# Optimization experiments

Hardware: AMD Instinct MI355X
Metric: run time of the kernel (lower is better)

Reference implementation:

```python
import jax, jax.numpy as jnp
import numpy as np

LN_EPS = 1e-5

def _dwconv(x, w, b, pad, groups):
    # x: (B,C,H,W), w: (C_out, C_in/groups, kh, kw)
    y = jax.lax.conv_general_dilated(
        x, w, window_strides=(1, 1),
        padding=[(pad[0], pad[0]), (pad[1], pad[1])],
        dimension_numbers=('NCHW', 'OIHW', 'NCHW'),
        feature_group_count=groups)
    return y + b[None, :, None, None]

def _ln(x, g, b):
    m = x.mean(-1, keepdims=True)
    v = ((x - m) ** 2).mean(-1, keepdims=True)
    return (x - m) / jnp.sqrt(v + LN_EPS) * g + b

def _lin(x, w, b):
    return x @ w.T + b

def setup_inputs() -> dict:
    key = jax.random.key(0)
    ks = jax.random.split(key, 24)
    f32 = jnp.float32
    W = lambda k, s: (jax.random.normal(k, s, f32) * 0.02)
    inp = {
        'feat': jax.random.normal(ks[0], (16, 64, 256, 256), f32),
        'head': jax.random.normal(ks[1], (16, 1, 64), f32),
        'pred': jax.random.normal(ks[2], (16, 1, 128, 128), f32),
        # dwconv Conv2d(1,1,3,3)
        'dw_w': W(ks[3], (1, 1, 3, 3)), 'dw_b': jnp.zeros((1,), f32),
        # InceptionDWConv2d(64): gc=8
        'inc_hw_w': W(ks[4], (8, 1, 3, 3)), 'inc_hw_b': jnp.zeros((8,), f32),
        'inc_w_w': W(ks[5], (8, 1, 1, 11)), 'inc_w_b': jnp.zeros((8,), f32),
        'inc_h_w': W(ks[6], (8, 1, 11, 1)), 'inc_h_b': jnp.zeros((8,), f32),
        # linear layers
        'pt_w': W(ks[7], (128, 64)), 'pt_b': jnp.zeros((128,), f32),
        'ht_w': W(ks[8], (128, 64)), 'ht_b': jnp.zeros((128,), f32),
        'pg_w': W(ks[9], (64, 64)), 'pg_b': jnp.zeros((64,), f32),
        'hg_w': W(ks[10], (64, 64)), 'hg_b': jnp.zeros((64,), f32),
        'fc_w': W(ks[11], (64, 64)), 'fc_b': jnp.zeros((64,), f32),
        # layernorms
        'pni_g': jnp.ones((64,), f32), 'pni_b': jnp.zeros((64,), f32),
        'hni_g': jnp.ones((64,), f32), 'hni_b': jnp.zeros((64,), f32),
        'pno_g': jnp.ones((64,), f32), 'pno_b': jnp.zeros((64,), f32),
        'hno_g': jnp.ones((64,), f32), 'hno_b': jnp.zeros((64,), f32),
        'fcn_g': jnp.ones((64,), f32), 'fcn_b': jnp.zeros((64,), f32),
    }
    return inp

def reference(feat, head, pred,
              dw_w, dw_b, inc_hw_w, inc_hw_b, inc_w_w, inc_w_b, inc_h_w, inc_h_b,
              pt_w, pt_b, ht_w, ht_b, pg_w, pg_b, hg_w, hg_b, fc_w, fc_b,
              pni_g, pni_b, hni_g, hni_b, pno_g, pno_b, hno_g, hno_b, fcn_g, fcn_b):
    bs, num_classes = head.shape[:2]
    C = 64  # in_channels == feat_channels
    B, _, Hp, Wp = pred.shape
    H, Wd = 2 * Hp, 2 * Wp
    # bilinear upsample x2 (align_corners=False == half-pixel)
    pred = jax.image.resize(pred, (B, num_classes, H, Wd), method='bilinear')
    pred = jax.nn.sigmoid(pred)
    pred_minus = 1.0 - jax.nn.sigmoid(pred)  # sigmoid applied twice, as in source
    pred_add = pred * pred_minus + pred
    pred_conv = _dwconv(pred_add, dw_w, dw_b, (1, 1), groups=1)
    pred = pred + pred_conv
    # InceptionDWConv2d: split (40,8,8,8)
    x_id, x_hw, x_w, x_h = feat[:, :40], feat[:, 40:48], feat[:, 48:56], feat[:, 56:64]
    feat = jnp.concatenate([
        x_id,
        _dwconv(x_hw, inc_hw_w, inc_hw_b, (1, 1), groups=8),
        _dwconv(x_w, inc_w_w, inc_w_b, (0, 5), groups=8),
        _dwconv(x_h, inc_h_w, inc_h_b, (5, 0), groups=8),
    ], axis=1)
    # FFT-based assembly: (bs,nc,1,H,W) x (bs,1,C,H,W)
    pred_fft = jnp.fft.rfft2(pred[:, :, None])
    feat_fft = jnp.fft.rfft2(feat[:, None])
    assemble = jnp.fft.irfft2(pred_fft * feat_fft, s=(H, Wd))  # (bs,nc,C,H,W)
    assemble = assemble.sum(axis=(3, 4))  # (bs,nc,C)
    # head: (bs,nc,C*k*k) -> (bs,nc,k*k,C)
    head = head.reshape(bs, num_classes, C, -1).transpose(0, 1, 3, 2)
    assemble = assemble.reshape(-1, C)
    bs_num = assemble.shape[0]
    pred_feat = _lin(assemble, pt_w, pt_b)  # (bs_num, 128)
    pred_feat_in = pred_feat[:, :C]
    pred_feat_out = pred_feat[:, -C:]
    head_feat = _lin(head.reshape(bs_num, -1, C), ht_w, ht_b)  # (bs_num, kk, 128)
    head_feat_in = head_feat[..., :C]
    head_feat_out = head_feat[..., -C:]
    gate_feat = head_feat_in * pred_feat_in[:, None, :]
    head_gate = jax.nn.sigmoid(_ln(_lin(gate_feat, hg_w, hg_b), hni_g, hni_b))
    pred_gate = jax.nn.sigmoid(_ln(_lin(gate_feat, pg_w, pg_b), pni_g, pni_b))
    head_feat_out = _ln(head_feat_out, hno_g, hno_b)
    pred_feat_out = _ln(pred_feat_out, pno_g, pno_b)
    update_head = pred_gate * pred_feat_out[:, None, :] + head_gate * head_feat_out
    update_head = _lin(update_head, fc_w, fc_b)
    update_head = jax.nn.relu(_ln(update_head, fcn_g, fcn_b))
    update_head = update_head.reshape(bs, num_classes, -1, C).transpose(0, 1, 3, 2)
    return update_head.reshape(bs, num_classes, C, 1, 1)
```

## Files before the change

kernel.cpp:

```cpp
#include <hip/hip_runtime.h>
#include <math.h>


typedef float nfloat4 __attribute__((ext_vector_type(4)));

__global__ __launch_bounds__(256) void k_main(
    const float* __restrict__ feat,
    const float* __restrict__ pred,
    const float* __restrict__ w_hw, const float* __restrict__ b_hw,
    const float* __restrict__ w_w,  const float* __restrict__ b_w,
    const float* __restrict__ w_h,  const float* __restrict__ b_h,
    float* __restrict__ sumF,
    float* __restrict__ predpart)
{
  const int tid  = threadIdx.x;
  const int lane = tid & 63;
  const int wid  = tid >> 6;

  if (blockIdx.x >= 128) {
    const int plane = blockIdx.x - 128;
    const int c = plane & 63;
    const nfloat4* x4 = reinterpret_cast<const nfloat4*>(feat) + (size_t)plane * 16384;

    if (c < 40) {
      __shared__ float red[4];
      float ax = 0.f, ay = 0.f, az = 0.f, aw = 0.f;
      #pragma unroll 8
      for (int it = 0; it < 64; ++it) {
        const nfloat4 v = __builtin_nontemporal_load(&x4[it * 256 + tid]);
        ax += v.x; ay += v.y; az += v.z; aw += v.w;
      }
      float tot = (ax + ay) + (az + aw);
      #pragma unroll
      for (int off = 32; off; off >>= 1) tot += __shfl_down(tot, off, 64);
      if (lane == 0) red[wid] = tot;
      __syncthreads();
      if (tid == 0) sumF[plane] = (red[0] + red[1]) + (red[2] + red[3]);
      return;
    }

    __shared__ float s_red[4];
    __shared__ float s_rs[10];
    __shared__ float s_cs4[4][10];
    __shared__ float s_k[4];

    float ax = 0.f, ay = 0.f, az = 0.f, aw = 0.f;
    float rowA = 0.f, rowB = 0.f, rowC = 0.f, rowD = 0.f;
    float v0x = 0.f, v0w = 0.f, v63x = 0.f, v63w = 0.f;
    #pragma unroll 8
    for (int it = 0; it < 64; ++it) {
      const nfloat4 v = __builtin_nontemporal_load(&x4[it * 256 + tid]);
      ax += v.x; ay += v.y; az += v.z; aw += v.w;
      const float s4 = (v.x + v.y) + (v.z + v.w);
      rowA += (it == 0)  ? s4 : 0.f;
      rowB += (it == 1)  ? s4 : 0.f;
      rowC += (it == 62) ? s4 : 0.f;
      rowD += (it == 63) ? s4 : 0.f;
      if (it == 0)  { v0x = v.x;  v0w = v.w; }
      if (it == 63) { v63x = v.x; v63w = v.w; }
    }
    float tot = (ax + ay) + (az + aw);
    float r0 = rowA, r1 = rowB, r2 = rowC, r3 = rowD;
    #pragma unroll
    for (int off = 32; off; off >>= 1) {
      tot += __shfl_down(tot, off, 64);
      r0  += __shfl_down(r0, off, 64);
      r1  += __shfl_down(r1, off, 64);
      r2  += __shfl_down(r2, off, 64);
      r3  += __shfl_down(r3, off, 64);
    }
    if (lane == 0) {
      s_red[wid] = tot;
      s_rs[wid] = r0;
      if (wid == 0) s_rs[4] = r1;
      if (wid == 3) s_rs[5] = r2;
      s_rs[6 + wid] = r3;
      s_cs4[wid][0] = ax; s_cs4[wid][1] = ay; s_cs4[wid][2] = az; s_cs4[wid][3] = aw;
    }
    if (lane == 1)  { s_cs4[wid][4] = ax; }
    if (lane == 62) { s_cs4[wid][5] = aw; }
    if (lane == 63) { s_cs4[wid][6] = ax; s_cs4[wid][7] = ay;
                      s_cs4[wid][8] = az; s_cs4[wid][9] = aw; }
    if (tid == 0)   s_k[0] = v0x;
    if (tid == 63)  s_k[1] = v0w;
    if (tid == 192) s_k[2] = v63x;
    if (tid == 255) s_k[3] = v63w;
    __syncthreads();

    if (tid == 0) {
      const float T = (s_red[0] + s_red[1]) + (s_red[2] + s_red[3]);
      float cs[10];
      #pragma unroll
      for (int k = 0; k < 10; ++k)
        cs[k] = (s_cs4[0][k] + s_cs4[1][k]) + (s_cs4[2][k] + s_cs4[3][k]);
      const float k00 = s_k[0], k01 = s_k[1], k10 = s_k[2], k11 = s_k[3];

      float topP[6], botP[6], leftP[6], rightP[6];
      topP[0] = botP[0] = leftP[0] = rightP[0] = 0.f;
      #pragma unroll
      for (int k = 0; k < 5; ++k) {
        topP[k+1]   = topP[k]   + s_rs[k];
        botP[k+1]   = botP[k]   + s_rs[9-k];
        leftP[k+1]  = leftP[k]  + cs[k];
        rightP[k+1] = rightP[k] + cs[9-k];
      }
      auto rect = [&](int du, int dv) -> float {
        float r = T;
        if (du > 0) r -= topP[du]; else if (du < 0) r -= botP[-du];
        if (dv > 0) r -= leftP[dv]; else if (dv < 0) r -= rightP[-dv];
        if (du > 0 && dv > 0) r += k00;
        else if (du > 0 && dv < 0) r += k01;
        else if (du < 0 && dv > 0) r += k10;
        else if (du < 0 && dv < 0) r += k11;
        return r;
      };
      float S;
      if (c < 48) {
        const int g = c - 40; const float* w = w_hw + g * 9;
        S = 65536.f * b_hw[g];
        #pragma unroll
        for (int u = 0; u < 3; ++u)
          #pragma unroll
          for (int v = 0; v < 3; ++v)
            S += w[u*3+v] * rect(u-1, v-1);
      } else if (c < 56) {
        const int g = c - 48; const float* w = w_w + g * 11;
        S = 65536.f * b_w[g];
        #pragma unroll
        for (int v = 0; v < 11; ++v) S += w[v] * rect(0, v-5);
      } else {
        const int g = c - 56; const float* w = w_h + g * 11;
        S = 65536.f * b_h[g];
        #pragma unroll
        for (int u = 0; u < 11; ++u) S += w[u] * rect(u-5, 0);
      }
      sumF[plane] = S;
    }
    return;
  }

  __shared__ float red[12];
  const int pb = blockIdx.x;
  const int b  = pb >> 3;
  const int g  = pb & 7;
  const int j  = tid;
  const float* src = pred + (size_t)b * 16384;

  const int kj = j >> 1;
  int c0, c1; float wc0, wc1;
  if ((j & 1) == 0) { c0 = (kj > 0) ? kj - 1 : 0; c1 = kj; wc0 = 0.25f; wc1 = 0.75f; }
  else              { c0 = kj; c1 = (kj < 127) ? kj + 1 : 127; wc0 = 0.75f; wc1 = 0.25f; }

  float accP = 0.f, accT = 0.f, accC = 0.f, redge = 0.f, cornA = 0.f, cornB = 0.f;
  const int i0 = g * 32;
  #pragma unroll 4
  for (int i = i0; i < i0 + 32; ++i) {
    const int ki = i >> 1;
    int r0, r1; float wr0, wr1;
    if ((i & 1) == 0) { r0 = (ki > 0) ? ki - 1 : 0; r1 = ki; wr0 = 0.25f; wr1 = 0.75f; }
    else              { r0 = ki; r1 = (ki < 127) ? ki + 1 : 127; wr0 = 0.75f; wr1 = 0.25f; }
    const float v = wr0 * (wc0 * src[r0*128 + c0] + wc1 * src[r0*128 + c1])
                  + wr1 * (wc0 * src[r1*128 + c0] + wc1 * src[r1*128 + c1]);
    const float p  = 1.f / (1.f + expf(-v));
    const float pm = 1.f - 1.f / (1.f + expf(-p));
    const float pa = p * pm + p;
    accP += p; accT += pa;
    if (j == 0 || j == 255) accC += pa;
    if (i == 0 || i == 255) {
      redge += pa;
      if (j == 0)   cornA = pa;
      if (j == 255) cornB = pa;
    }
  }
  float a0 = accP, a1 = accT, a2 = redge;
  #pragma unroll
  for (int off = 32; off; off >>= 1) {
    a0 += __shfl_down(a0, off, 64);
    a1 += __shfl_down(a1, off, 64);
    a2 += __shfl_down(a2, off, 64);
  }
  if (lane == 0) { red[wid] = a0; red[4 + wid] = a1; red[8 + wid] = a2; }
  __syncthreads();
  float* pp = predpart + pb * 8;
  if (tid == 0) {
    pp[0] = (red[0] + red[1]) + (red[2] + red[3]);
    pp[1] = (red[4] + red[5]) + (red[6] + red[7]);
    pp[4] = (red[8] + red[9]) + (red[10] + red[11]);
    pp[2] = accC; pp[5] = cornA;
  }
  if (tid == 255) { pp[3] = accC; pp[6] = cornB; }
}

__device__ __forceinline__ float wsum64(float v) {
  #pragma unroll
  for (int off = 32; off; off >>= 1) v += __shfl_xor(v, off, 64);
  return v;
}

__global__ __launch_bounds__(128) void k_tail(
    const float* __restrict__ sumF, const float* __restrict__ predpart,
    const float* __restrict__ head,
    const float* __restrict__ dw_w, const float* __restrict__ dw_b,
    const float* __restrict__ pt_w, const float* __restrict__ pt_b,
    const float* __restrict__ ht_w, const float* __restrict__ ht_b,
    const float* __restrict__ pg_w, const float* __restrict__ pg_b,
    const float* __restrict__ hg_w, const float* __restrict__ hg_b,
    const float* __restrict__ fc_w, const float* __restrict__ fc_b,
    const float* __restrict__ pni_g, const float* __restrict__ pni_b,
    const float* __restrict__ hni_g, const float* __restrict__ hni_b,
    const float* __restrict__ pno_g, const float* __restrict__ pno_b,
    const float* __restrict__ hno_g, const float* __restrict__ hno_b,
    const float* __restrict__ fcn_g, const float* __restrict__ fcn_b,
    float* __restrict__ out)
{
  const int b = blockIdx.x;
  const int t = threadIdx.x;
  const int ln = t & 63;
  __shared__ float a[64], hd[64], pf[128], hf[128], gate[64];
  __shared__ float hgate[64], pgate[64], pfo[64], hfo[64], upd[64];
  __shared__ float s_sP;

  const float sf = (t < 64) ? sumF[b * 64 + t] : 0.f;
  if (t < 64) hd[t] = head[b * 64 + t];

  if (t == 0) {
    const float* pp = predpart + b * 64;
    float P = 0.f, T = 0.f, C0 = 0.f, C255 = 0.f;
    #pragma unroll
    for (int g = 0; g < 8; ++g) {
      P += pp[g*8 + 0]; T += pp[g*8 + 1]; C0 += pp[g*8 + 2]; C255 += pp[g*8 + 3];
    }
    const float R0 = pp[0*8 + 4], R255 = pp[7*8 + 4];
    const float k00 = pp[0*8 + 5], k01 = pp[0*8 + 6];
    const float k10 = pp[7*8 + 5], k11 = pp[7*8 + 6];
    auto rect = [&](int du, int dv) -> float {
      float r = T;
      if (du > 0) r -= R0; else if (du < 0) r -= R255;
      if (dv > 0) r -= C0; else if (dv < 0) r -= C255;
      if (du > 0 && dv > 0) r += k00;
      else if (du > 0 && dv < 0) r += k01;
      else if (du < 0 && dv > 0) r += k10;
      else if (du < 0 && dv < 0) r += k11;
      return r;
    };
    float S = P + 65536.f * dw_b[0];
    #pragma unroll
    for (int u = 0; u < 3; ++u)
      #pragma unroll
      for (int v = 0; v < 3; ++v)
        S += dw_w[u*3+v] * rect(u-1, v-1);
    s_sP = S;
  }
  __syncthreads();
  if (t < 64) a[t] = sf * s_sP;
  __syncthreads();

  {
    const float4* ptw4 = reinterpret_cast<const float4*>(pt_w) + t * 16;
    const float4* htw4 = reinterpret_cast<const float4*>(ht_w) + t * 16;
    const float4* a4  = reinterpret_cast<const float4*>(a);
    const float4* hd4 = reinterpret_cast<const float4*>(hd);
    float sp = pt_b[t], sh = ht_b[t];
    #pragma unroll
    for (int kk = 0; kk < 16; ++kk) {
      const float4 wp = ptw4[kk], wh = htw4[kk];
      const float4 av = a4[kk],  hv = hd4[kk];
      sp += av.x*wp.x + av.y*wp.y + av.z*wp.z + av.w*wp.w;
      sh += hv.x*wh.x + hv.y*wh.y + hv.z*wh.z + hv.w*wh.w;
    }
    pf[t] = sp; hf[t] = sh;
  }
  __syncthreads();
  if (t < 64) gate[t] = hf[t] * pf[t];
  __syncthreads();

  float glin;
  {
    const float* gw = (t < 64) ? hg_w : pg_w;
    float s = (t < 64) ? hg_b[ln] : pg_b[ln];
    const float4* gw4 = reinterpret_cast<const float4*>(gw) + ln * 16;
    const float4* g4  = reinterpret_cast<const float4*>(gate);
    #pragma unroll
    for (int kk = 0; kk < 16; ++kk) {
      const float4 w = gw4[kk], gv = g4[kk];
      s += gv.x*w.x + gv.y*w.y + gv.z*w.z + gv.w*w.w;
    }
    glin = s;
  }
  {
    const float m = wsum64(glin) * (1.f/64.f);
    const float d = glin - m;
    const float var = wsum64(d*d) * (1.f/64.f);
    const float* g  = (t < 64) ? hni_g : pni_g;
    const float* bb = (t < 64) ? hni_b : pni_b;
    const float y = d / sqrtf(var + 1e-5f) * g[ln] + bb[ln];
    const float sg = 1.f / (1.f + expf(-y));
    if (t < 64) hgate[ln] = sg; else pgate[ln] = sg;
  }
  {
    const float x = (t < 64) ? hf[64 + ln] : pf[64 + ln];
    const float m = wsum64(x) * (1.f/64.f);
    const float d = x - m;
    const float var = wsum64(d*d) * (1.f/64.f);
    const float* g  = (t < 64) ? hno_g : pno_g;
    const float* bb = (t < 64) ? hno_b : pno_b;
    const float y = d / sqrtf(var + 1e-5f) * g[ln] + bb[ln];
    if (t < 64) hfo[ln] = y; else pfo[ln] = y;
  }
  __syncthreads();
  if (t < 64) upd[t] = pgate[t] * pfo[t] + hgate[t] * hfo[t];
  __syncthreads();
  if (t < 64) {
    const float4* fw4 = reinterpret_cast<const float4*>(fc_w) + t * 16;
    const float4* u4  = reinterpret_cast<const float4*>(upd);
    float s = fc_b[t];
    #pragma unroll
    for (int kk = 0; kk < 16; ++kk) {
      const float4 w = fw4[kk], uv = u4[kk];
      s += uv.x*w.x + uv.y*w.y + uv.z*w.z + uv.w*w.w;
    }
    const float m = wsum64(s) * (1.f/64.f);
    const float d = s - m;
    const float var = wsum64(d*d) * (1.f/64.f);
    const float y = d / sqrtf(var + 1e-5f) * fcn_g[t] + fcn_b[t];
    out[b * 64 + t] = fmaxf(y, 0.f);
  }
}

extern "C" void kernel_launch(void* const* d_in, const int* in_sizes, int n_in,
                              void* d_out, int out_size, void* d_ws, size_t ws_size,
                              hipStream_t stream) {
  (void)in_sizes; (void)n_in; (void)out_size; (void)ws_size;
  const float* feat     = (const float*)d_in[0];
  const float* head     = (const float*)d_in[1];
  const float* pred     = (const float*)d_in[2];
  const float* dw_w     = (const float*)d_in[3];
  const float* dw_b     = (const float*)d_in[4];
  const float* inc_hw_w = (const float*)d_in[5];
  const float* inc_hw_b = (const float*)d_in[6];
  const float* inc_w_w  = (const float*)d_in[7];
  const float* inc_w_b  = (const float*)d_in[8];
  const float* inc_h_w  = (const float*)d_in[9];
  const float* inc_h_b  = (const float*)d_in[10];
  const float* pt_w  = (const float*)d_in[11];
  const float* pt_b  = (const float*)d_in[12];
  const float* ht_w  = (const float*)d_in[13];
  const float* ht_b  = (const float*)d_in[14];
  const float* pg_w  = (const float*)d_in[15];
  const float* pg_b  = (const float*)d_in[16];
  const float* hg_w  = (const float*)d_in[17];
  const float* hg_b  = (const float*)d_in[18];
  const float* fc_w  = (const float*)d_in[19];
  const float* fc_b  = (const float*)d_in[20];
  const float* pni_g = (const float*)d_in[21];
  const float* pni_b = (const float*)d_in[22];
  const float* hni_g = (const float*)d_in[23];
  const float* hni_b = (const float*)d_in[24];
  const float* pno_g = (const float*)d_in[25];
  const float* pno_b = (const float*)d_in[26];
  const float* hno_g = (const float*)d_in[27];
  const float* hno_b = (const float*)d_in[28];
  const float* fcn_g = (const float*)d_in[29];
  const float* fcn_b = (const float*)d_in[30];

  float* out      = (float*)d_out;
  float* sumF     = (float*)d_ws;
  float* predpart = sumF + 1024;

  k_main<<<1152, 256, 0, stream>>>(feat, pred,
                                   inc_hw_w, inc_hw_b, inc_w_w, inc_w_b,
                                   inc_h_w, inc_h_b, sumF, predpart);
  k_tail<<<16, 128, 0, stream>>>(sumF, predpart, head, dw_w, dw_b,
                                 pt_w, pt_b, ht_w, ht_b,
                                 pg_w, pg_b, hg_w, hg_b, fc_w, fc_b,
                                 pni_g, pni_b, hni_g, hni_b,
                                 pno_g, pno_b, hno_g, hno_b,
                                 fcn_g, fcn_b, out);
}
```

Measured before the change: 53.66 us.

## Fuse tail into main kernel via per-batch last-block-done atomic counter

Merges the two kernels into one launch. Each block increments a per-batch counter when it finishes, and the last of the 72 blocks for that batch runs the small MLP tail, reading partial results with atomic loads. This removes the second kernel launch and the gap between kernels. In exchange it adds a memset launch for the counters, atomics and fences in every block, and the tail now runs serially at the end of the last block for each batch.

```diff
diff --git a/kernel.cpp b/kernel.cpp
--- a/kernel.cpp
+++ b/kernel.cpp
@@ -4,201 +4,22 @@
 
 typedef float nfloat4 __attribute__((ext_vector_type(4)));
 
-__global__ __launch_bounds__(256) void k_main(
+__device__ __forceinline__ float aload(const float* p) {
+  return __hip_atomic_load(p, __ATOMIC_RELAXED, __HIP_MEMORY_SCOPE_AGENT);
+}
+
+__device__ __forceinline__ float wsum64(float v) {
+  #pragma unroll
+  for (int off = 32; off; off >>= 1) v += __shfl_xor(v, off, 64);
+  return v;
+}
+
+__global__ __launch_bounds__(256) void k_all(
     const float* __restrict__ feat,
     const float* __restrict__ pred,
     const float* __restrict__ w_hw, const float* __restrict__ b_hw,
     const float* __restrict__ w_w,  const float* __restrict__ b_w,
     const float* __restrict__ w_h,  const float* __restrict__ b_h,
-    float* __restrict__ sumF,
-    float* __restrict__ predpart)
-{
-  const int tid  = threadIdx.x;
-  const int lane = tid & 63;
-  const int wid  = tid >> 6;
-
-  if (blockIdx.x >= 128) {
-    const int plane = blockIdx.x - 128;
-    const int c = plane & 63;
-    const nfloat4* x4 = reinterpret_cast<const nfloat4*>(feat) + (size_t)plane * 16384;
-
-    if (c < 40) {
-      __shared__ float red[4];
-      float ax = 0.f, ay = 0.f, az = 0.f, aw = 0.f;
-      #pragma unroll 8
-      for (int it = 0; it < 64; ++it) {
-        const nfloat4 v = __builtin_nontemporal_load(&x4[it * 256 + tid]);
-        ax += v.x; ay += v.y; az += v.z; aw += v.w;
-      }
-      float tot = (ax + ay) + (az + aw);
-      #pragma unroll
-      for (int off = 32; off; off >>= 1) tot += __shfl_down(tot, off, 64);
-      if (lane == 0) red[wid] = tot;
-      __syncthreads();
-      if (tid == 0) sumF[plane] = (red[0] + red[1]) + (red[2] + red[3]);
-      return;
-    }
-
-    __shared__ float s_red[4];
-    __shared__ float s_rs[10];
-    __shared__ float s_cs4[4][10];
-    __shared__ float s_k[4];
-
-    float ax = 0.f, ay = 0.f, az = 0.f, aw = 0.f;
-    float rowA = 0.f, rowB = 0.f, rowC = 0.f, rowD = 0.f;
-    float v0x = 0.f, v0w = 0.f, v63x = 0.f, v63w = 0.f;
-    #pragma unroll 8
-    for (int it = 0; it < 64; ++it) {
-      const nfloat4 v = __builtin_nontemporal_load(&x4[it * 256 + tid]);
-      ax += v.x; ay += v.y; az += v.z; aw += v.w;
-      const float s4 = (v.x + v.y) + (v.z + v.w);
-      rowA += (it == 0)  ? s4 : 0.f;
-      rowB += (it == 1)  ? s4 : 0.f;
-      rowC += (it == 62) ? s4 : 0.f;
-      rowD += (it == 63) ? s4 : 0.f;
-      if (it == 0)  { v0x = v.x;  v0w = v.w; }
-      if (it == 63) { v63x = v.x; v63w = v.w; }
-    }
-    float tot = (ax + ay) + (az + aw);
-    float r0 = rowA, r1 = rowB, r2 = rowC, r3 = rowD;
-    #pragma unroll
-    for (int off = 32; off; off >>= 1) {
-      tot += __shfl_down(tot, off, 64);
-      r0  += __shfl_down(r0, off, 64);
-      r1  += __shfl_down(r1, off, 64);
-      r2  += __shfl_down(r2, off, 64);
-      r3  += __shfl_down(r3, off, 64);
-    }
-    if (lane == 0) {
-      s_red[wid] = tot;
-      s_rs[wid] = r0;
-      if (wid == 0) s_rs[4] = r1;
-      if (wid == 3) s_rs[5] = r2;
-      s_rs[6 + wid] = r3;
-      s_cs4[wid][0] = ax; s_cs4[wid][1] = ay; s_cs4[wid][2] = az; s_cs4[wid][3] = aw;
-    }
-    if (lane == 1)  { s_cs4[wid][4] = ax; }
-    if (lane == 62) { s_cs4[wid][5] = aw; }
-    if (lane == 63) { s_cs4[wid][6] = ax; s_cs4[wid][7] = ay;
-                      s_cs4[wid][8] = az; s_cs4[wid][9] = aw; }
-    if (tid == 0)   s_k[0] = v0x;
-    if (tid == 63)  s_k[1] = v0w;
-    if (tid == 192) s_k[2] = v63x;
-    if (tid == 255) s_k[3] = v63w;
-    __syncthreads();
-
-    if (tid == 0) {
-      const float T = (s_red[0] + s_red[1]) + (s_red[2] + s_red[3]);
-      float cs[10];
-      #pragma unroll
-      for (int k = 0; k < 10; ++k)
-        cs[k] = (s_cs4[0][k] + s_cs4[1][k]) + (s_cs4[2][k] + s_cs4[3][k]);
-      const float k00 = s_k[0], k01 = s_k[1], k10 = s_k[2], k11 = s_k[3];
-
-      float topP[6], botP[6], leftP[6], rightP[6];
-      topP[0] = botP[0] = leftP[0] = rightP[0] = 0.f;
-      #pragma unroll
-      for (int k = 0; k < 5; ++k) {
-        topP[k+1]   = topP[k]   + s_rs[k];
-        botP[k+1]   = botP[k]   + s_rs[9-k];
-        leftP[k+1]  = leftP[k]  + cs[k];
-        rightP[k+1] = rightP[k] + cs[9-k];
-      }
-      auto rect = [&](int du, int dv) -> float {
-        float r = T;
-        if (du > 0) r -= topP[du]; else if (du < 0) r -= botP[-du];
-        if (dv > 0) r -= leftP[dv]; else if (dv < 0) r -= rightP[-dv];
-        if (du > 0 && dv > 0) r += k00;
-        else if (du > 0 && dv < 0) r += k01;
-        else if (du < 0 && dv > 0) r += k10;
-        else if (du < 0 && dv < 0) r += k11;
-        return r;
-      };
-      float S;
-      if (c < 48) {
-        const int g = c - 40; const float* w = w_hw + g * 9;
-        S = 65536.f * b_hw[g];
-        #pragma unroll
-        for (int u = 0; u < 3; ++u)
-          #pragma unroll
-          for (int v = 0; v < 3; ++v)
-            S += w[u*3+v] * rect(u-1, v-1);
-      } else if (c < 56) {
-        const int g = c - 48; const float* w = w_w + g * 11;
-        S = 65536.f * b_w[g];
-        #pragma unroll
-        for (int v = 0; v < 11; ++v) S += w[v] * rect(0, v-5);
-      } else {
-        const int g = c - 56; const float* w = w_h + g * 11;
-        S = 65536.f * b_h[g];
-        #pragma unroll
-        for (int u = 0; u < 11; ++u) S += w[u] * rect(u-5, 0);
-      }
-      sumF[plane] = S;
-    }
-    return;
-  }
-
-  __shared__ float red[12];
-  const int pb = blockIdx.x;
-  const int b  = pb >> 3;
-  const int g  = pb & 7;
-  const int j  = tid;
-  const float* src = pred + (size_t)b * 16384;
-
-  const int kj = j >> 1;
-  int c0, c1; float wc0, wc1;
-  if ((j & 1) == 0) { c0 = (kj > 0) ? kj - 1 : 0; c1 = kj; wc0 = 0.25f; wc1 = 0.75f; }
-  else              { c0 = kj; c1 = (kj < 127) ? kj + 1 : 127; wc0 = 0.75f; wc1 = 0.25f; }
-
-  float accP = 0.f, accT = 0.f, accC = 0.f, redge = 0.f, cornA = 0.f, cornB = 0.f;
-  const int i0 = g * 32;
-  #pragma unroll 4
-  for (int i = i0; i < i0 + 32; ++i) {
-    const int ki = i >> 1;
-    int r0, r1; float wr0, wr1;
-    if ((i & 1) == 0) { r0 = (ki > 0) ? ki - 1 : 0; r1 = ki; wr0 = 0.25f; wr1 = 0.75f; }
-    else              { r0 = ki; r1 = (ki < 127) ? ki + 1 : 127; wr0 = 0.75f; wr1 = 0.25f; }
-    const float v = wr0 * (wc0 * src[r0*128 + c0] + wc1 * src[r0*128 + c1])
-                  + wr1 * (wc0 * src[r1*128 + c0] + wc1 * src[r1*128 + c1]);
-    const float p  = 1.f / (1.f + expf(-v));
-    const float pm = 1.f - 1.f / (1.f + expf(-p));
-    const float pa = p * pm + p;
-    accP += p; accT += pa;
-    if (j == 0 || j == 255) accC += pa;
-    if (i == 0 || i == 255) {
-      redge += pa;
-      if (j == 0)   cornA = pa;
-      if (j == 255) cornB = pa;
-    }
-  }
-  float a0 = accP, a1 = accT, a2 = redge;
-  #pragma unroll
-  for (int off = 32; off; off >>= 1) {
-    a0 += __shfl_down(a0, off, 64);
-    a1 += __shfl_down(a1, off, 64);
-    a2 += __shfl_down(a2, off, 64);
-  }
-  if (lane == 0) { red[wid] = a0; red[4 + wid] = a1; red[8 + wid] = a2; }
-  __syncthreads();
-  float* pp = predpart + pb * 8;
-  if (tid == 0) {
-    pp[0] = (red[0] + red[1]) + (red[2] + red[3]);
-    pp[1] = (red[4] + red[5]) + (red[6] + red[7]);
-    pp[4] = (red[8] + red[9]) + (red[10] + red[11]);
-    pp[2] = accC; pp[5] = cornA;
-  }
-  if (tid == 255) { pp[3] = accC; pp[6] = cornB; }
-}
-
-__device__ __forceinline__ float wsum64(float v) {
-  #pragma unroll
-  for (int off = 32; off; off >>= 1) v += __shfl_xor(v, off, 64);
-  return v;
-}
-
-__global__ __launch_bounds__(128) void k_tail(
-    const float* __restrict__ sumF, const float* __restrict__ predpart,
     const float* __restrict__ head,
     const float* __restrict__ dw_w, const float* __restrict__ dw_b,
     const float* __restrict__ pt_w, const float* __restrict__ pt_b,
@@ -211,28 +32,224 @@
     const float* __restrict__ pno_g, const float* __restrict__ pno_b,
     const float* __restrict__ hno_g, const float* __restrict__ hno_b,
     const float* __restrict__ fcn_g, const float* __restrict__ fcn_b,
+    float* __restrict__ sumF,
+    float* __restrict__ predpart,
+    int*   __restrict__ cnt,
     float* __restrict__ out)
 {
-  const int b = blockIdx.x;
-  const int t = threadIdx.x;
-  const int ln = t & 63;
+  const int tid  = threadIdx.x;
+  const int lane = tid & 63;
+  const int wid  = tid >> 6;
+  int b;
+
+  if (blockIdx.x < 1024) {
+    const int plane = blockIdx.x;
+    b = plane >> 6;
+    const int c = plane & 63;
+    const nfloat4* x4 = reinterpret_cast<const nfloat4*>(feat) + (size_t)plane * 16384;
+
+    if (c < 40) {
+      __shared__ float red_i[4];
+      float ax = 0.f, ay = 0.f, az = 0.f, aw = 0.f;
+      #pragma unroll 8
+      for (int it = 0; it < 64; ++it) {
+        const nfloat4 v = __builtin_nontemporal_load(&x4[it * 256 + tid]);
+        ax += v.x; ay += v.y; az += v.z; aw += v.w;
+      }
+      float tot = (ax + ay) + (az + aw);
+      #pragma unroll
+      for (int off = 32; off; off >>= 1) tot += __shfl_down(tot, off, 64);
+      if (lane == 0) red_i[wid] = tot;
+      __syncthreads();
+      if (tid == 0) sumF[plane] = (red_i[0] + red_i[1]) + (red_i[2] + red_i[3]);
+    } else {
+      __shared__ float s_red[4];
+      __shared__ float s_rs[10];
+      __shared__ float s_cs4[4][10];
+      __shared__ float s_k[4];
+
+      float ax = 0.f, ay = 0.f, az = 0.f, aw = 0.f;
+      float rowA = 0.f, rowB = 0.f, rowC = 0.f, rowD = 0.f;
+      float v0x = 0.f, v0w = 0.f, v63x = 0.f, v63w = 0.f;
+      #pragma unroll 8
+      for (int it = 0; it < 64; ++it) {
+        const nfloat4 v = __builtin_nontemporal_load(&x4[it * 256 + tid]);
+        ax += v.x; ay += v.y; az += v.z; aw += v.w;
+        const float s4 = (v.x + v.y) + (v.z + v.w);
+        rowA += (it == 0)  ? s4 : 0.f;
+        rowB += (it == 1)  ? s4 : 0.f;
+        rowC += (it == 62) ? s4 : 0.f;
+        rowD += (it == 63) ? s4 : 0.f;
+        if (it == 0)  { v0x = v.x;  v0w = v.w; }
+        if (it == 63) { v63x = v.x; v63w = v.w; }
+      }
+      float tot = (ax + ay) + (az + aw);
+      float r0 = rowA, r1 = rowB, r2 = rowC, r3 = rowD;
+      #pragma unroll
+      for (int off = 32; off; off >>= 1) {
+        tot += __shfl_down(tot, off, 64);
+        r0  += __shfl_down(r0, off, 64);
+        r1  += __shfl_down(r1, off, 64);
+        r2  += __shfl_down(r2, off, 64);
+        r3  += __shfl_down(r3, off, 64);
+      }
+      if (lane == 0) {
+        s_red[wid] = tot;
+        s_rs[wid] = r0;
+        if (wid == 0) s_rs[4] = r1;
+        if (wid == 3) s_rs[5] = r2;
+        s_rs[6 + wid] = r3;
+        s_cs4[wid][0] = ax; s_cs4[wid][1] = ay; s_cs4[wid][2] = az; s_cs4[wid][3] = aw;
+      }
+      if (lane == 1)  { s_cs4[wid][4] = ax; }
+      if (lane == 62) { s_cs4[wid][5] = aw; }
+      if (lane == 63) { s_cs4[wid][6] = ax; s_cs4[wid][7] = ay;
+                        s_cs4[wid][8] = az; s_cs4[wid][9] = aw; }
+      if (tid == 0)   s_k[0] = v0x;
+      if (tid == 63)  s_k[1] = v0w;
+      if (tid == 192) s_k[2] = v63x;
+      if (tid == 255) s_k[3] = v63w;
+      __syncthreads();
+
+      if (tid == 0) {
+        const float T = (s_red[0] + s_red[1]) + (s_red[2] + s_red[3]);
+        float cs[10];
+        #pragma unroll
+        for (int k = 0; k < 10; ++k)
+          cs[k] = (s_cs4[0][k] + s_cs4[1][k]) + (s_cs4[2][k] + s_cs4[3][k]);
+        const float k00 = s_k[0], k01 = s_k[1], k10 = s_k[2], k11 = s_k[3];
+
+        float topP[6], botP[6], leftP[6], rightP[6];
+        topP[0] = botP[0] = leftP[0] = rightP[0] = 0.f;
+        #pragma unroll
+        for (int k = 0; k < 5; ++k) {
+          topP[k+1]   = topP[k]   + s_rs[k];
+          botP[k+1]   = botP[k]   + s_rs[9-k];
+          leftP[k+1]  = leftP[k]  + cs[k];
+          rightP[k+1] = rightP[k] + cs[9-k];
+        }
+        auto rect = [&](int du, int dv) -> float {
+          float r = T;
+          if (du > 0) r -= topP[du]; else if (du < 0) r -= botP[-du];
+          if (dv > 0) r -= leftP[dv]; else if (dv < 0) r -= rightP[-dv];
+          if (du > 0 && dv > 0) r += k00;
+          else if (du > 0 && dv < 0) r += k01;
+          else if (du < 0 && dv > 0) r += k10;
+          else if (du < 0 && dv < 0) r += k11;
+          return r;
+        };
+        float S;
+        if (c < 48) {
+          const int g = c - 40; const float* w = w_hw + g * 9;
+          S = 65536.f * b_hw[g];
+          #pragma unroll
+          for (int u = 0; u < 3; ++u)
+            #pragma unroll
+            for (int v = 0; v < 3; ++v)
+              S += w[u*3+v] * rect(u-1, v-1);
+        } else if (c < 56) {
+          const int g = c - 48; const float* w = w_w + g * 11;
+          S = 65536.f * b_w[g];
+          #pragma unroll
+          for (int v = 0; v < 11; ++v) S += w[v] * rect(0, v-5);
+        } else {
+          const int g = c - 56; const float* w = w_h + g * 11;
+          S = 65536.f * b_h[g];
+          #pragma unroll
+          for (int u = 0; u < 11; ++u) S += w[u] * rect(u-5, 0);
+        }
+        sumF[plane] = S;
+      }
+    }
+  } else {
+    __shared__ float red[12];
+    __shared__ float s_edge[3];
+    const int pb = blockIdx.x - 1024;
+    b = pb >> 3;
+    const int g  = pb & 7;
+    const int j  = tid;
+    const float* src = pred + (size_t)b * 16384;
+
+    const int kj = j >> 1;
+    int c0, c1; float wc0, wc1;
+    if ((j & 1) == 0) { c0 = (kj > 0) ? kj - 1 : 0; c1 = kj; wc0 = 0.25f; wc1 = 0.75f; }
+    else              { c0 = kj; c1 = (kj < 127) ? kj + 1 : 127; wc0 = 0.75f; wc1 = 0.25f; }
+
+    float accP = 0.f, accT = 0.f, accC = 0.f, redge = 0.f, cornA = 0.f, cornB = 0.f;
+    const int i0 = g * 32;
+    #pragma unroll 4
+    for (int i = i0; i < i0 + 32; ++i) {
+      const int ki = i >> 1;
+      int r0, r1; float wr0, wr1;
+      if ((i & 1) == 0) { r0 = (ki > 0) ? ki - 1 : 0; r1 = ki; wr0 = 0.25f; wr1 = 0.75f; }
+      else              { r0 = ki; r1 = (ki < 127) ? ki + 1 : 127; wr0 = 0.75f; wr1 = 0.25f; }
+      const float v = wr0 * (wc0 * src[r0*128 + c0] + wc1 * src[r0*128 + c1])
+                    + wr1 * (wc0 * src[r1*128 + c0] + wc1 * src[r1*128 + c1]);
+      const float p  = 1.f / (1.f + expf(-v));
+      const float pm = 1.f - 1.f / (1.f + expf(-p));
+      const float pa = p * pm + p;
+      accP += p; accT += pa;
+      if (j == 0 || j == 255) accC += pa;
+      if (i == 0 || i == 255) {
+        redge += pa;
+        if (j == 0)   cornA = pa;
+        if (j == 255) cornB = pa;
+      }
+    }
+    if (j == 255) { s_edge[0] = accC; s_edge[1] = cornB; }
+    float a0 = accP, a1 = accT, a2 = redge;
+    #pragma unroll
+    for (int off = 32; off; off >>= 1) {
+      a0 += __shfl_down(a0, off, 64);
+      a1 += __shfl_down(a1, off, 64);
+      a2 += __shfl_down(a2, off, 64);
+    }
+    if (lane == 0) { red[wid] = a0; red[4 + wid] = a1; red[8 + wid] = a2; }
+    __syncthreads();
+    if (tid == 0) {
+      float* pp = predpart + pb * 8;
+      pp[0] = (red[0] + red[1]) + (red[2] + red[3]);
+      pp[1] = (red[4] + red[5]) + (red[6] + red[7]);
+      pp[4] = (red[8] + red[9]) + (red[10] + red[11]);
+      pp[2] = accC; pp[5] = cornA;
+      pp[3] = s_edge[0]; pp[6] = s_edge[1];
+    }
+  }
+
+  __shared__ int s_do_tail;
+  __syncthreads();
+  if (tid == 0) {
+    __threadfence();
+    const int old = __hip_atomic_fetch_add(&cnt[b], 1, __ATOMIC_ACQ_REL,
+                                           __HIP_MEMORY_SCOPE_AGENT);
+    s_do_tail = (old == 71) ? 1 : 0;
+  }
+  __syncthreads();
+  if (!s_do_tail) return;
+
+  const int t = tid, ln = t & 63;
   __shared__ float a[64], hd[64], pf[128], hf[128], gate[64];
   __shared__ float hgate[64], pgate[64], pfo[64], hfo[64], upd[64];
+  __shared__ float s_pp[64];
   __shared__ float s_sP;
 
-  const float sf = (t < 64) ? sumF[b * 64 + t] : 0.f;
-  if (t < 64) hd[t] = head[b * 64 + t];
+  float sf = 0.f;
+  if (t < 64) {
+    sf      = aload(&sumF[b * 64 + t]);
+    s_pp[t] = aload(&predpart[b * 64 + t]);
+    hd[t]   = head[b * 64 + t];
+  }
+  __syncthreads();
 
   if (t == 0) {
-    const float* pp = predpart + b * 64;
     float P = 0.f, T = 0.f, C0 = 0.f, C255 = 0.f;
     #pragma unroll
     for (int g = 0; g < 8; ++g) {
-      P += pp[g*8 + 0]; T += pp[g*8 + 1]; C0 += pp[g*8 + 2]; C255 += pp[g*8 + 3];
-    }
-    const float R0 = pp[0*8 + 4], R255 = pp[7*8 + 4];
-    const float k00 = pp[0*8 + 5], k01 = pp[0*8 + 6];
-    const float k10 = pp[7*8 + 5], k11 = pp[7*8 + 6];
+      P += s_pp[g*8 + 0]; T += s_pp[g*8 + 1]; C0 += s_pp[g*8 + 2]; C255 += s_pp[g*8 + 3];
+    }
+    const float R0 = s_pp[0*8 + 4], R255 = s_pp[7*8 + 4];
+    const float k00 = s_pp[0*8 + 5], k01 = s_pp[0*8 + 6];
+    const float k10 = s_pp[7*8 + 5], k11 = s_pp[7*8 + 6];
     auto rect = [&](int du, int dv) -> float {
       float r = T;
       if (du > 0) r -= R0; else if (du < 0) r -= R255;
@@ -255,7 +272,7 @@
   if (t < 64) a[t] = sf * s_sP;
   __syncthreads();
 
-  {
+  if (t < 128) {
     const float4* ptw4 = reinterpret_cast<const float4*>(pt_w) + t * 16;
     const float4* htw4 = reinterpret_cast<const float4*>(ht_w) + t * 16;
     const float4* a4  = reinterpret_cast<const float4*>(a);
@@ -274,38 +291,40 @@
   if (t < 64) gate[t] = hf[t] * pf[t];
   __syncthreads();
 
-  float glin;
-  {
-    const float* gw = (t < 64) ? hg_w : pg_w;
-    float s = (t < 64) ? hg_b[ln] : pg_b[ln];
-    const float4* gw4 = reinterpret_cast<const float4*>(gw) + ln * 16;
-    const float4* g4  = reinterpret_cast<const float4*>(gate);
-    #pragma unroll
-    for (int kk = 0; kk < 16; ++kk) {
-      const float4 w = gw4[kk], gv = g4[kk];
-      s += gv.x*w.x + gv.y*w.y + gv.z*w.z + gv.w*w.w;
-    }
-    glin = s;
-  }
-  {
-    const float m = wsum64(glin) * (1.f/64.f);
-    const float d = glin - m;
-    const float var = wsum64(d*d) * (1.f/64.f);
-    const float* g  = (t < 64) ? hni_g : pni_g;
-    const float* bb = (t < 64) ? hni_b : pni_b;
-    const float y = d / sqrtf(var + 1e-5f) * g[ln] + bb[ln];
-    const float sg = 1.f / (1.f + expf(-y));
-    if (t < 64) hgate[ln] = sg; else pgate[ln] = sg;
-  }
-  {
-    const float x = (t < 64) ? hf[64 + ln] : pf[64 + ln];
-    const float m = wsum64(x) * (1.f/64.f);
-    const float d = x - m;
-    const float var = wsum64(d*d) * (1.f/64.f);
-    const float* g  = (t < 64) ? hno_g : pno_g;
-    const float* bb = (t < 64) ? hno_b : pno_b;
-    const float y = d / sqrtf(var + 1e-5f) * g[ln] + bb[ln];
-    if (t < 64) hfo[ln] = y; else pfo[ln] = y;
+  if (t < 128) {
+    float glin;
+    {
+      const float* gw = (t < 64) ? hg_w : pg_w;
+      float s = (t < 64) ? hg_b[ln] : pg_b[ln];
+      const float4* gw4 = reinterpret_cast<const float4*>(gw) + ln * 16;
+      const float4* g4  = reinterpret_cast<const float4*>(gate);
+      #pragma unroll
+      for (int kk = 0; kk < 16; ++kk) {
+        const float4 w = gw4[kk], gv = g4[kk];
+        s += gv.x*w.x + gv.y*w.y + gv.z*w.z + gv.w*w.w;
+      }
+      glin = s;
+    }
+    {
+      const float m = wsum64(glin) * (1.f/64.f);
+      const float d = glin - m;
+      const float var = wsum64(d*d) * (1.f/64.f);
+      const float* gg = (t < 64) ? hni_g : pni_g;
+      const float* bb = (t < 64) ? hni_b : pni_b;
+      const float y = d / sqrtf(var + 1e-5f) * gg[ln] + bb[ln];
+      const float sg = 1.f / (1.f + expf(-y));
+      if (t < 64) hgate[ln] = sg; else pgate[ln] = sg;
+    }
+    {
+      const float x = (t < 64) ? hf[64 + ln] : pf[64 + ln];
+      const float m = wsum64(x) * (1.f/64.f);
+      const float d = x - m;
+      const float var = wsum64(d*d) * (1.f/64.f);
+      const float* gg = (t < 64) ? hno_g : pno_g;
+      const float* bb = (t < 64) ? hno_b : pno_b;
+      const float y = d / sqrtf(var + 1e-5f) * gg[ln] + bb[ln];
+      if (t < 64) hfo[ln] = y; else pfo[ln] = y;
+    }
   }
   __syncthreads();
   if (t < 64) upd[t] = pgate[t] * pfo[t] + hgate[t] * hfo[t];
@@ -366,14 +385,18 @@
   float* out      = (float*)d_out;
   float* sumF     = (float*)d_ws;
   float* predpart = sumF + 1024;
-
-  k_main<<<1152, 256, 0, stream>>>(feat, pred,
-                                   inc_hw_w, inc_hw_b, inc_w_w, inc_w_b,
-                                   inc_h_w, inc_h_b, sumF, predpart);
-  k_tail<<<16, 128, 0, stream>>>(sumF, predpart, head, dw_w, dw_b,
-                                 pt_w, pt_b, ht_w, ht_b,
-                                 pg_w, pg_b, hg_w, hg_b, fc_w, fc_b,
-                                 pni_g, pni_b, hni_g, hni_b,
-                                 pno_g, pno_b, hno_g, hno_b,
-                                 fcn_g, fcn_b, out);
+  int*   cnt      = (int*)((char*)d_ws + 8192);
+
+  hipMemsetAsync(cnt, 0, 16 * sizeof(int), stream);
+
+  k_all<<<1152, 256, 0, stream>>>(feat, pred,
+                                  inc_hw_w, inc_hw_b, inc_w_w, inc_w_b,
+                                  inc_h_w, inc_h_b,
+                                  head, dw_w, dw_b,
+                                  pt_w, pt_b, ht_w, ht_b,
+                                  pg_w, pg_b, hg_w, hg_b, fc_w, fc_b,
+                                  pni_g, pni_b, hni_g, hni_b,
+                                  pno_g, pno_b, hno_g, hno_b,
+                                  fcn_g, fcn_b,
+                                  sumF, predpart, cnt, out);
 }
```

New measurement: 151.4 us. 182% more time.
